# Performance work log

Measured on AMD Instinct MI355X. Metric: run time of the kernel, lower is better.

The kernel has to match this reference:

```python
import jax, jax.numpy as jnp
import numpy as np

B, S, HID, ENC = 64, 1024, 1024, 2048
NEG = -1e10

def setup_inputs() -> dict:
    key = jax.random.key(0)
    k1, k2, k3, k4, k5 = jax.random.split(key, 5)
    decoder_hidden = jax.random.normal(k1, (B, HID), dtype=jnp.float32)
    encoder_outputs = jax.random.normal(k2, (B, S, ENC), dtype=jnp.float32)
    mask = jnp.ones((B, S), dtype=jnp.int32)
    # learned params (torch nn.Linear weight layout: [out, in]; no bias)
    Wq = jax.random.normal(k3, (HID, HID), dtype=jnp.float32) / np.sqrt(HID)
    Wk = jax.random.normal(k4, (HID, ENC), dtype=jnp.float32) / np.sqrt(ENC)
    v = jax.random.normal(k5, (HID,), dtype=jnp.float32) / np.sqrt(HID)
    return {"decoder_hidden": decoder_hidden, "encoder_outputs": encoder_outputs,
            "mask": mask, "Wq": Wq, "Wk": Wk, "v": v}

def reference(decoder_hidden, encoder_outputs, mask, Wq, Wk, v):
    # query: [B, 1, HID]
    query = (decoder_hidden @ Wq.T)[:, None, :]
    # keys: [B, S, HID]
    keys = jnp.einsum('bse,he->bsh', encoder_outputs, Wk)
    # energy: [B, S]  (v-projection of tanh(query + keys))
    energy = jnp.einsum('bsh,h->bs', jnp.tanh(query + keys), v)
    energy = jnp.where(mask == 0, jnp.float32(NEG), energy)
    attn_weights = jax.nn.softmax(energy, axis=1)
    # context: [B, ENC]
    context = jnp.einsum('bs,bse->be', attn_weights, encoder_outputs)
    return context, attn_weights
```

## Files before the change

kernel.cpp:

```cpp
#include <hip/hip_runtime.h>
#include <hip/hip_bf16.h>


#define B_   64
#define S_   1024
#define HID_ 1024
#define ENC_ 2048

typedef unsigned short u16;
typedef float  f32x4  __attribute__((ext_vector_type(4)));
typedef __bf16 bf16x8 __attribute__((ext_vector_type(8)));
typedef u16    u16x8  __attribute__((ext_vector_type(8)));

__device__ __forceinline__ u16 f2bf(float f) {
    unsigned u = __float_as_uint(f);
    u += 0x7FFFu + ((u >> 16) & 1u);
    return (u16)(u >> 16);
}
__device__ __forceinline__ float bf2f(u16 h) {
    return __uint_as_float(((unsigned)h) << 16);
}

__device__ __forceinline__ void gload16(const void* g, void* l) {
    __builtin_amdgcn_global_load_lds(
        (const __attribute__((address_space(1))) unsigned int*)g,
        (__attribute__((address_space(3))) unsigned int*)l,
        16, 0, 0);
}

#define BAR() __builtin_amdgcn_s_barrier()
#define LG0() do { asm volatile("s_waitcnt lgkmcnt(0)" ::: "memory"); \
                   __builtin_amdgcn_sched_barrier(0); } while (0)
#define VM4() asm volatile("s_waitcnt vmcnt(4)" ::: "memory")

__global__ __launch_bounds__(256) void cvt_kernel(const float* __restrict__ in,
                                                  u16* __restrict__ out, long n8) {
    long stride = (long)gridDim.x * blockDim.x;
    for (long i = (long)blockIdx.x * blockDim.x + threadIdx.x; i < n8; i += stride) {
        const float4* p = (const float4*)(in + (i << 3));
        float4 a = p[0], c = p[1];
        u16x8 o;
        o[0] = f2bf(a.x); o[1] = f2bf(a.y); o[2] = f2bf(a.z); o[3] = f2bf(a.w);
        o[4] = f2bf(c.x); o[5] = f2bf(c.y); o[6] = f2bf(c.z); o[7] = f2bf(c.w);
        *(u16x8*)(out + (i << 3)) = o;
    }
}

__global__ __launch_bounds__(256) void query_kernel(const float* __restrict__ dh,
                                                    const float* __restrict__ Wq,
                                                    float* __restrict__ q) {
    int w = threadIdx.x >> 6, l = threadIdx.x & 63;
    int h = (blockIdx.x << 2) + w;
    float4 wv[4];
    const float* wrow = Wq + (size_t)h * HID_;
    #pragma unroll
    for (int it = 0; it < 4; ++it) wv[it] = *(const float4*)(wrow + (it << 8) + (l << 2));
    for (int b = 0; b < 64; ++b) {
        const float* dr = dh + (b << 10);
        float s = 0.f;
        #pragma unroll
        for (int it = 0; it < 4; ++it) {
            float4 d = *(const float4*)(dr + (it << 8) + (l << 2));
            s += wv[it].x * d.x + wv[it].y * d.y + wv[it].z * d.z + wv[it].w * d.w;
        }
        #pragma unroll
        for (int off = 32; off >= 1; off >>= 1) s += __shfl_xor(s, off);
        if (l == 0) q[(b << 10) + h] = s;
    }
}

__global__ __launch_bounds__(512, 2) void keys_gemm(const u16* __restrict__ A,
                                                    const u16* __restrict__ Bw,
                                                    const float* __restrict__ q,
                                                    const float* __restrict__ v,
                                                    float* __restrict__ energy) {
    __shared__ char smem[131072];
    int bid = blockIdx.x;
    int wg = ((bid & 7) << 7) + (bid >> 3);
    int mt = wg >> 2, nt = wg & 3;
    int t = threadIdx.x;
    int w = t >> 6, l = t & 63;
    int wm = w >> 2, wn = w & 3;
    int lhi = l >> 4, llo = l & 15;
    const u16* Apan = A  + ((size_t)mt << 8) * ENC_;
    const u16* Bpan = Bw + ((size_t)nt << 8) * ENC_;

    int r0 = t >> 3, g0 = t & 7;
    int r1 = (512 + t) >> 3, g1 = t & 7;
    int c0 = (g0 ^ (r0 & 7)) << 3;
    int c1 = (g1 ^ (r1 & 7)) << 3;

    char* aHalf = smem + wm * 16384;
    char* bHalf = smem + 32768 + (wn >> 1) * 16384;
    int bRowO = (wn & 1) << 6;
    int axor = (llo & 7) << 4;

    f32x4 acc[8][4] = {};
    bf16x8 a[4][2], b01[2][2], b23[2][2];

    auto STAGE = [&](const u16* pan, int rowBase, int kt, int ldsOfs) {
        gload16(pan + (size_t)(rowBase + r0) * ENC_ + kt + c0, smem + ldsOfs + (t << 4));
        gload16(pan + (size_t)(rowBase + r1) * ENC_ + kt + c1, smem + ldsOfs + 8192 + (t << 4));
    };
    auto LDA = [&](int bufofs, int ibase) {
        #pragma unroll
        for (int ii = 0; ii < 4; ++ii)
            #pragma unroll
            for (int k = 0; k < 2; ++k)
                a[ii][k] = *(const bf16x8*)(aHalf + bufofs +
                    ((llo + ((ibase + ii) << 4)) << 7) + ((((k << 2) + lhi) << 4) ^ axor));
    };
    auto LDB = [&](bf16x8 (&bb)[2][2], int bufofs, int jbase) {
        #pragma unroll
        for (int j = 0; j < 2; ++j)
            #pragma unroll
            for (int k = 0; k < 2; ++k)
                bb[j][k] = *(const bf16x8*)(bHalf + bufofs +
                    ((bRowO + llo + ((jbase + j) << 4)) << 7) + ((((k << 2) + lhi) << 4) ^ axor));
    };
    auto MM = [&](bf16x8 (&bb)[2][2], int ibase, int jbase) {
        __builtin_amdgcn_s_setprio(1);
        #pragma unroll
        for (int ii = 0; ii < 4; ++ii)
            #pragma unroll
            for (int j = 0; j < 2; ++j)
                #pragma unroll
                for (int k = 0; k < 2; ++k)
                    acc[ibase + ii][jbase + j] = __builtin_amdgcn_mfma_f32_16x16x32_bf16(
                        a[ii][k], bb[j][k], acc[ibase + ii][jbase + j], 0, 0, 0);
        __builtin_amdgcn_s_setprio(0);
    };

    STAGE(Apan, 0,   0,  0);
    STAGE(Apan, 128, 0,  16384);
    STAGE(Bpan, 0,   0,  32768);
    STAGE(Bpan, 128, 0,  49152);
    STAGE(Bpan, 0,   64, 65536 + 32768);
    STAGE(Bpan, 128, 64, 65536 + 49152);
    VM4();
    BAR();

    #pragma unroll 1
    for (int u = 0; u < 16; ++u) {
        int ktA = u << 7, ktB = ktA + 64;
        int ks2 = ktA + 128; if (ks2 >= ENC_) ks2 -= 128;
        int ks3 = ktA + 192; if (ks3 >= ENC_) ks3 -= 128;

        LDA(0, 0); LDB(b01, 0, 0);
        STAGE(Apan, 0, ktB, 65536);
        BAR(); LG0(); MM(b01, 0, 0); BAR();
        LDB(b23, 0, 2);
        STAGE(Apan, 128, ktB, 65536 + 16384);
        BAR(); LG0(); MM(b23, 0, 2); BAR();
        LDA(0, 4);
        STAGE(Bpan, 0, ks2, 32768);
        BAR(); LG0(); MM(b23, 4, 2); BAR();
        STAGE(Bpan, 128, ks2, 49152);
        VM4();
        BAR(); LG0(); MM(b01, 4, 0); BAR();
        LDA(65536, 0); LDB(b01, 65536, 0);
        STAGE(Apan, 0, ks2, 0);
        BAR(); LG0(); MM(b01, 0, 0); BAR();
        LDB(b23, 65536, 2);
        STAGE(Apan, 128, ks2, 16384);
        BAR(); LG0(); MM(b23, 0, 2); BAR();
        LDA(65536, 4);
        STAGE(Bpan, 0, ks3, 65536 + 32768);
        BAR(); LG0(); MM(b23, 4, 2); BAR();
        STAGE(Bpan, 128, ks3, 65536 + 49152);
        VM4();
        BAR(); LG0(); MM(b01, 4, 0); BAR();
    }

    int b = mt >> 2;
    float qv[4], vv[4];
    #pragma unroll
    for (int j = 0; j < 4; ++j) {
        int h = (nt << 8) + (wn << 6) + (j << 4) + llo;
        qv[j] = q[(b << 10) + h];
        vv[j] = v[h];
    }
    #pragma unroll
    for (int i = 0; i < 8; ++i) {
        #pragma unroll
        for (int r = 0; r < 4; ++r) {
            float part = 0.f;
            #pragma unroll
            for (int j = 0; j < 4; ++j)
                part += tanhf(qv[j] + acc[i][j][r]) * vv[j];
            part += __shfl_down(part, 8);
            part += __shfl_down(part, 4);
            part += __shfl_down(part, 2);
            part += __shfl_down(part, 1);
            if (llo == 0) {
                int m = (mt << 8) + (wm << 7) + (i << 4) + (lhi << 2) + r;
                atomicAdd(&energy[m], part);
            }
        }
    }
}

__global__ __launch_bounds__(256) void softmax_kernel(const float* __restrict__ energy,
                                                      const int* __restrict__ mask,
                                                      float* __restrict__ attn) {
    int b = blockIdx.x, t = threadIdx.x;
    int w = t >> 6, l = t & 63;
    __shared__ float rmax[4], rsum[4];
    float4 e = *(const float4*)(energy + (b << 10) + (t << 2));
    int4 mk = *(const int4*)(mask + (b << 10) + (t << 2));
    if (mk.x == 0) e.x = -1e10f;
    if (mk.y == 0) e.y = -1e10f;
    if (mk.z == 0) e.z = -1e10f;
    if (mk.w == 0) e.w = -1e10f;
    float mx = fmaxf(fmaxf(e.x, e.y), fmaxf(e.z, e.w));
    for (int off = 32; off >= 1; off >>= 1) mx = fmaxf(mx, __shfl_xor(mx, off));
    if (l == 0) rmax[w] = mx;
    __syncthreads();
    mx = fmaxf(fmaxf(rmax[0], rmax[1]), fmaxf(rmax[2], rmax[3]));
    float4 ex;
    ex.x = expf(e.x - mx); ex.y = expf(e.y - mx);
    ex.z = expf(e.z - mx); ex.w = expf(e.w - mx);
    float sm = ex.x + ex.y + ex.z + ex.w;
    for (int off = 32; off >= 1; off >>= 1) sm += __shfl_xor(sm, off);
    if (l == 0) rsum[w] = sm;
    __syncthreads();
    sm = rsum[0] + rsum[1] + rsum[2] + rsum[3];
    float inv = 1.0f / sm;
    ex.x *= inv; ex.y *= inv; ex.z *= inv; ex.w *= inv;
    *(float4*)(attn + (b << 10) + (t << 2)) = ex;
}

__global__ __launch_bounds__(256) void context_kernel(const u16* __restrict__ enc_bf,
                                                      const float* __restrict__ attn,
                                                      float* __restrict__ ctx) {
    int b = blockIdx.y;
    int s0 = blockIdx.x << 7;
    int t = threadIdx.x;
    int e0 = t << 3;
    float acc[8] = {};
    const u16* base = enc_bf + ((size_t)((b << 10) + s0)) * ENC_ + e0;
    const float* wp = attn + (b << 10) + s0;
    for (int s = 0; s < 128; ++s) {
        float wgt = wp[s];
        u16x8 u = *(const u16x8*)(base + (size_t)s * ENC_);
        #pragma unroll
        for (int k = 0; k < 8; ++k) acc[k] += wgt * bf2f(u[k]);
    }
    float* cb = ctx + (b << 11) + e0;
    #pragma unroll
    for (int k = 0; k < 8; ++k) atomicAdd(&cb[k], acc[k]);
}

extern "C" void kernel_launch(void* const* d_in, const int* in_sizes, int n_in,
                              void* d_out, int out_size, void* d_ws, size_t ws_size,
                              hipStream_t stream) {
    const float* dh   = (const float*)d_in[0];
    const float* enc  = (const float*)d_in[1];
    const int*   mask = (const int*)d_in[2];
    const float* Wq   = (const float*)d_in[3];
    const float* Wk   = (const float*)d_in[4];
    const float* v    = (const float*)d_in[5];
    float* out  = (float*)d_out;
    float* ctx  = out;
    float* attn = out + B_ * ENC_;

    const size_t ENC_BF_BYTES = (size_t)B_ * S_ * ENC_ * 2;
    const size_t WK_BF_BYTES  = (size_t)HID_ * ENC_ * 2;
    const size_t Q_BYTES      = (size_t)B_ * HID_ * 4;
    const size_t E_BYTES      = (size_t)B_ * S_ * 4;
    if (ws_size < ENC_BF_BYTES + WK_BF_BYTES + Q_BYTES + E_BYTES) return;

    char* ws = (char*)d_ws;
    u16*   enc_bf = (u16*)ws;
    u16*   wk_bf  = (u16*)(ws + ENC_BF_BYTES);
    float* qbuf   = (float*)(ws + ENC_BF_BYTES + WK_BF_BYTES);
    float* energy = (float*)(ws + ENC_BF_BYTES + WK_BF_BYTES + Q_BYTES);

    hipMemsetAsync(energy, 0, E_BYTES, stream);
    hipMemsetAsync(d_out, 0, (size_t)out_size * 4, stream);

    cvt_kernel<<<2048, 256, 0, stream>>>(enc, enc_bf, (long)((size_t)B_ * S_ * ENC_ / 8));
    cvt_kernel<<<128, 256, 0, stream>>>(Wk, wk_bf, (long)((size_t)HID_ * ENC_ / 8));
    query_kernel<<<256, 256, 0, stream>>>(dh, Wq, qbuf);
    keys_gemm<<<1024, 512, 0, stream>>>(enc_bf, wk_bf, qbuf, v, energy);
    softmax_kernel<<<B_, 256, 0, stream>>>(energy, mask, attn);
    context_kernel<<<dim3(8, B_), 256, 0, stream>>>(enc_bf, attn, ctx);
}
```

Before: 1.125 ms.

## Fuse fp32-to-bf16 encoder conversion into GEMM staging via register prefetch

```diff
diff --git a/kernel.cpp b/kernel.cpp
--- a/kernel.cpp
+++ b/kernel.cpp
@@ -17,21 +17,9 @@
     u += 0x7FFFu + ((u >> 16) & 1u);
     return (u16)(u >> 16);
 }
-__device__ __forceinline__ float bf2f(u16 h) {
-    return __uint_as_float(((unsigned)h) << 16);
-}
-
-__device__ __forceinline__ void gload16(const void* g, void* l) {
-    __builtin_amdgcn_global_load_lds(
-        (const __attribute__((address_space(1))) unsigned int*)g,
-        (__attribute__((address_space(3))) unsigned int*)l,
-        16, 0, 0);
-}
-
-#define BAR() __builtin_amdgcn_s_barrier()
-#define LG0() do { asm volatile("s_waitcnt lgkmcnt(0)" ::: "memory"); \
-                   __builtin_amdgcn_sched_barrier(0); } while (0)
-#define VM4() asm volatile("s_waitcnt vmcnt(4)" ::: "memory")
+
+#define BARM() asm volatile("s_barrier" ::: "memory")
+#define LGB()  asm volatile("s_waitcnt lgkmcnt(0)\n\ts_barrier" ::: "memory")
 
 __global__ __launch_bounds__(256) void cvt_kernel(const float* __restrict__ in,
                                                   u16* __restrict__ out, long n8) {
@@ -69,7 +57,7 @@
     }
 }
 
-__global__ __launch_bounds__(512, 2) void keys_gemm(const u16* __restrict__ A,
+__global__ __launch_bounds__(512, 2) void keys_gemm(const float* __restrict__ A,
                                                     const u16* __restrict__ Bw,
                                                     const float* __restrict__ q,
                                                     const float* __restrict__ v,
@@ -82,13 +70,12 @@
     int w = t >> 6, l = t & 63;
     int wm = w >> 2, wn = w & 3;
     int lhi = l >> 4, llo = l & 15;
-    const u16* Apan = A  + ((size_t)mt << 8) * ENC_;
-    const u16* Bpan = Bw + ((size_t)nt << 8) * ENC_;
-
-    int r0 = t >> 3, g0 = t & 7;
-    int r1 = (512 + t) >> 3, g1 = t & 7;
-    int c0 = (g0 ^ (r0 & 7)) << 3;
-    int c1 = (g1 ^ (r1 & 7)) << 3;
+    const float* Apan = A  + ((size_t)mt << 8) * ENC_;
+    const u16*   Bpan = Bw + ((size_t)nt << 8) * ENC_;
+
+    int r0 = t >> 3;
+    int r1 = 64 + r0;
+    int c0 = (((t & 7) ^ (r0 & 7)) << 3);
 
     char* aHalf = smem + wm * 16384;
     char* bHalf = smem + 32768 + (wn >> 1) * 16384;
@@ -96,12 +83,45 @@
     int axor = (llo & 7) << 4;
 
     f32x4 acc[8][4] = {};
-    bf16x8 a[4][2], b01[2][2], b23[2][2];
-
-    auto STAGE = [&](const u16* pan, int rowBase, int kt, int ldsOfs) {
-        gload16(pan + (size_t)(rowBase + r0) * ENC_ + kt + c0, smem + ldsOfs + (t << 4));
-        gload16(pan + (size_t)(rowBase + r1) * ENC_ + kt + c1, smem + ldsOfs + 8192 + (t << 4));
-    };
+    bf16x8 a[4][2], b01e[2][2], b01o[2][2], b23[2][2];
+
+    struct AFrag { float4 x0, x1, y0, y1; };
+    struct BFrag { u16x8 x, y; };
+    AFrag sA;
+    BFrag sB;
+
+    auto loadA = [&](int rowBase, int kt) -> AFrag {
+        const float* p0 = Apan + (size_t)(rowBase + r0) * ENC_ + kt + c0;
+        const float* p1 = Apan + (size_t)(rowBase + r1) * ENC_ + kt + c0;
+        AFrag f;
+        f.x0 = *(const float4*)p0; f.x1 = *(const float4*)(p0 + 4);
+        f.y0 = *(const float4*)p1; f.y1 = *(const float4*)(p1 + 4);
+        return f;
+    };
+    auto writeA = [&](const AFrag& f, int ldsOfs) {
+        bf16x8 o0, o1;
+        o0[0] = (__bf16)f.x0.x; o0[1] = (__bf16)f.x0.y;
+        o0[2] = (__bf16)f.x0.z; o0[3] = (__bf16)f.x0.w;
+        o0[4] = (__bf16)f.x1.x; o0[5] = (__bf16)f.x1.y;
+        o0[6] = (__bf16)f.x1.z; o0[7] = (__bf16)f.x1.w;
+        o1[0] = (__bf16)f.y0.x; o1[1] = (__bf16)f.y0.y;
+        o1[2] = (__bf16)f.y0.z; o1[3] = (__bf16)f.y0.w;
+        o1[4] = (__bf16)f.y1.x; o1[5] = (__bf16)f.y1.y;
+        o1[6] = (__bf16)f.y1.z; o1[7] = (__bf16)f.y1.w;
+        *(bf16x8*)(smem + ldsOfs + (t << 4)) = o0;
+        *(bf16x8*)(smem + ldsOfs + 8192 + (t << 4)) = o1;
+    };
+    auto loadB = [&](int rowBase, int kt) -> BFrag {
+        BFrag f;
+        f.x = *(const u16x8*)(Bpan + (size_t)(rowBase + r0) * ENC_ + kt + c0);
+        f.y = *(const u16x8*)(Bpan + (size_t)(rowBase + r1) * ENC_ + kt + c0);
+        return f;
+    };
+    auto writeB = [&](const BFrag& f, int ldsOfs) {
+        *(u16x8*)(smem + ldsOfs + (t << 4)) = f.x;
+        *(u16x8*)(smem + ldsOfs + 8192 + (t << 4)) = f.y;
+    };
+
     auto LDA = [&](int bufofs, int ibase) {
         #pragma unroll
         for (int ii = 0; ii < 4; ++ii)
@@ -118,7 +138,7 @@
                 bb[j][k] = *(const bf16x8*)(bHalf + bufofs +
                     ((bRowO + llo + ((jbase + j) << 4)) << 7) + ((((k << 2) + lhi) << 4) ^ axor));
     };
-    auto MM = [&](bf16x8 (&bb)[2][2], int ibase, int jbase) {
+    auto MMq = [&](bf16x8 (&bb)[2][2], int ibase, int jbase) {
         __builtin_amdgcn_s_setprio(1);
         #pragma unroll
         for (int ii = 0; ii < 4; ++ii)
@@ -131,14 +151,18 @@
         __builtin_amdgcn_s_setprio(0);
     };
 
-    STAGE(Apan, 0,   0,  0);
-    STAGE(Apan, 128, 0,  16384);
-    STAGE(Bpan, 0,   0,  32768);
-    STAGE(Bpan, 128, 0,  49152);
-    STAGE(Bpan, 0,   64, 65536 + 32768);
-    STAGE(Bpan, 128, 64, 65536 + 49152);
-    VM4();
-    BAR();
+    {
+        AFrag pA;
+        BFrag pB;
+        pA = loadA(0, 0);    writeA(pA, 0);
+        pA = loadA(128, 0);  writeA(pA, 16384);
+        pB = loadB(0, 0);    writeB(pB, 32768);
+        pB = loadB(128, 0);  writeB(pB, 49152);
+        pB = loadB(0, 64);   writeB(pB, 65536 + 32768);
+        sB = loadB(128, 64);
+    }
+    LGB();
+    LDB(b01e, 0, 0);
 
     #pragma unroll 1
     for (int u = 0; u < 16; ++u) {
@@ -146,30 +170,30 @@
         int ks2 = ktA + 128; if (ks2 >= ENC_) ks2 -= 128;
         int ks3 = ktA + 192; if (ks3 >= ENC_) ks3 -= 128;
 
-        LDA(0, 0); LDB(b01, 0, 0);
-        STAGE(Apan, 0, ktB, 65536);
-        BAR(); LG0(); MM(b01, 0, 0); BAR();
+        LDA(0, 0);
+        writeB(sB, 65536 + 49152);   sA = loadA(0, ktB);
+        BARM(); MMq(b01e, 0, 0); LGB();
         LDB(b23, 0, 2);
-        STAGE(Apan, 128, ktB, 65536 + 16384);
-        BAR(); LG0(); MM(b23, 0, 2); BAR();
+        writeA(sA, 65536);           sA = loadA(128, ktB);
+        BARM(); MMq(b23, 0, 2); LGB();
         LDA(0, 4);
-        STAGE(Bpan, 0, ks2, 32768);
-        BAR(); LG0(); MM(b23, 4, 2); BAR();
-        STAGE(Bpan, 128, ks2, 49152);
-        VM4();
-        BAR(); LG0(); MM(b01, 4, 0); BAR();
-        LDA(65536, 0); LDB(b01, 65536, 0);
-        STAGE(Apan, 0, ks2, 0);
-        BAR(); LG0(); MM(b01, 0, 0); BAR();
+        writeA(sA, 65536 + 16384);   sB = loadB(0, ks2);
+        BARM(); MMq(b23, 4, 2); LGB();
+        LDB(b01o, 65536, 0);
+        writeB(sB, 32768);           sB = loadB(128, ks2);
+        BARM(); MMq(b01e, 4, 0); LGB();
+        LDA(65536, 0);
+        writeB(sB, 49152);           sA = loadA(0, ks2);
+        BARM(); MMq(b01o, 0, 0); LGB();
         LDB(b23, 65536, 2);
-        STAGE(Apan, 128, ks2, 16384);
-        BAR(); LG0(); MM(b23, 0, 2); BAR();
+        writeA(sA, 0);               sA = loadA(128, ks2);
+        BARM(); MMq(b23, 0, 2); LGB();
         LDA(65536, 4);
-        STAGE(Bpan, 0, ks3, 65536 + 32768);
-        BAR(); LG0(); MM(b23, 4, 2); BAR();
-        STAGE(Bpan, 128, ks3, 65536 + 49152);
-        VM4();
-        BAR(); LG0(); MM(b01, 4, 0); BAR();
+        writeA(sA, 16384);           sB = loadB(0, ks3);
+        BARM(); MMq(b23, 4, 2); LGB();
+        LDB(b01e, 0, 0);
+        writeB(sB, 65536 + 32768);   sB = loadB(128, ks3);
+        BARM(); MMq(b01o, 4, 0); LGB();
     }
 
     int b = mt >> 2;
@@ -230,25 +254,28 @@
     *(float4*)(attn + (b << 10) + (t << 2)) = ex;
 }
 
-__global__ __launch_bounds__(256) void context_kernel(const u16* __restrict__ enc_bf,
+__global__ __launch_bounds__(256) void context_kernel(const float* __restrict__ enc,
                                                       const float* __restrict__ attn,
                                                       float* __restrict__ ctx) {
     int b = blockIdx.y;
     int s0 = blockIdx.x << 7;
     int t = threadIdx.x;
     int e0 = t << 3;
-    float acc[8] = {};
-    const u16* base = enc_bf + ((size_t)((b << 10) + s0)) * ENC_ + e0;
+    float4 a0 = {0.f, 0.f, 0.f, 0.f}, a1 = {0.f, 0.f, 0.f, 0.f};
+    const float* base = enc + ((size_t)((b << 10) + s0)) * ENC_ + e0;
     const float* wp = attn + (b << 10) + s0;
     for (int s = 0; s < 128; ++s) {
         float wgt = wp[s];
-        u16x8 u = *(const u16x8*)(base + (size_t)s * ENC_);
-        #pragma unroll
-        for (int k = 0; k < 8; ++k) acc[k] += wgt * bf2f(u[k]);
+        float4 u0 = *(const float4*)(base + (size_t)s * ENC_);
+        float4 u1 = *(const float4*)(base + (size_t)s * ENC_ + 4);
+        a0.x += wgt * u0.x; a0.y += wgt * u0.y; a0.z += wgt * u0.z; a0.w += wgt * u0.w;
+        a1.x += wgt * u1.x; a1.y += wgt * u1.y; a1.z += wgt * u1.z; a1.w += wgt * u1.w;
     }
     float* cb = ctx + (b << 11) + e0;
-    #pragma unroll
-    for (int k = 0; k < 8; ++k) atomicAdd(&cb[k], acc[k]);
+    atomicAdd(&cb[0], a0.x); atomicAdd(&cb[1], a0.y);
+    atomicAdd(&cb[2], a0.z); atomicAdd(&cb[3], a0.w);
+    atomicAdd(&cb[4], a1.x); atomicAdd(&cb[5], a1.y);
+    atomicAdd(&cb[6], a1.z); atomicAdd(&cb[7], a1.w);
 }
 
 extern "C" void kernel_launch(void* const* d_in, const int* in_sizes, int n_in,
@@ -264,25 +291,22 @@
     float* ctx  = out;
     float* attn = out + B_ * ENC_;
 
-    const size_t ENC_BF_BYTES = (size_t)B_ * S_ * ENC_ * 2;
     const size_t WK_BF_BYTES  = (size_t)HID_ * ENC_ * 2;
     const size_t Q_BYTES      = (size_t)B_ * HID_ * 4;
     const size_t E_BYTES      = (size_t)B_ * S_ * 4;
-    if (ws_size < ENC_BF_BYTES + WK_BF_BYTES + Q_BYTES + E_BYTES) return;
+    if (ws_size < WK_BF_BYTES + Q_BYTES + E_BYTES) return;
 
     char* ws = (char*)d_ws;
-    u16*   enc_bf = (u16*)ws;
-    u16*   wk_bf  = (u16*)(ws + ENC_BF_BYTES);
-    float* qbuf   = (float*)(ws + ENC_BF_BYTES + WK_BF_BYTES);
-    float* energy = (float*)(ws + ENC_BF_BYTES + WK_BF_BYTES + Q_BYTES);
+    u16*   wk_bf  = (u16*)ws;
+    float* qbuf   = (float*)(ws + WK_BF_BYTES);
+    float* energy = (float*)(ws + WK_BF_BYTES + Q_BYTES);
 
     hipMemsetAsync(energy, 0, E_BYTES, stream);
     hipMemsetAsync(d_out, 0, (size_t)out_size * 4, stream);
 
-    cvt_kernel<<<2048, 256, 0, stream>>>(enc, enc_bf, (long)((size_t)B_ * S_ * ENC_ / 8));
     cvt_kernel<<<128, 256, 0, stream>>>(Wk, wk_bf, (long)((size_t)HID_ * ENC_ / 8));
     query_kernel<<<256, 256, 0, stream>>>(dh, Wq, qbuf);
-    keys_gemm<<<1024, 512, 0, stream>>>(enc_bf, wk_bf, qbuf, v, energy);
+    keys_gemm<<<1024, 512, 0, stream>>>(enc, wk_bf, qbuf, v, energy);
     softmax_kernel<<<B_, 256, 0, stream>>>(energy, mask, attn);
-    context_kernel<<<dim3(8, B_), 256, 0, stream>>>(enc_bf, attn, ctx);
-}
+    context_kernel<<<dim3(8, B_), 256, 0, stream>>>(enc, attn, ctx);
+}
```

Result: slower. 1.254 ms (+11.4%).
